# Kernel optimization log

Hardware: AMD Instinct MI355X
Metric: run time of the kernel (lower is better)

The kernel has to match this reference:

```python
import jax, jax.numpy as jnp
import numpy as np
from jax import lax

HID = 2048; NK = 16; NV = 32; DK = 128; DV = 128; KSZ = 4; CHUNK = 64; S = 2048
KEY_DIM = NK * DK; VAL_DIM = NV * DV; CONV_DIM = 2 * KEY_DIM + VAL_DIM
EPS = 1e-6


def l2norm(x, eps=1e-6):
    return x * lax.rsqrt((x * x).sum(-1, keepdims=True) + eps)


def chunk_gated_delta_rule(q, k, v, g, beta, chunk=CHUNK):
    # q,k: [B,S,Hv,DK]; v: [B,S,Hv,DV]; g,beta: [B,S,Hv]
    q = l2norm(q); k = l2norm(k)  # use_qk_l2norm_in_kernel=True
    q, k, v = (jnp.swapaxes(x, 1, 2) for x in (q, k, v))  # [B,H,S,D]
    g = jnp.swapaxes(g, 1, 2); beta = jnp.swapaxes(beta, 1, 2)  # [B,H,S]
    B, H, Ssz, Dk = k.shape; Dv = v.shape[-1]
    N = Ssz // chunk  # seq_len chosen divisible by chunk -> pad is no-op
    q = q * (Dk ** -0.5)
    vb = v * beta[..., None]
    kb = k * beta[..., None]
    rs = lambda x: x.reshape(B, H, N, chunk, x.shape[-1])
    q, k, v, kb, vb = map(rs, (q, k, v, kb, vb))
    g = jnp.cumsum(g.reshape(B, H, N, chunk), axis=-1)
    tril = jnp.tril(jnp.ones((chunk, chunk), bool))
    stril = jnp.tril(jnp.ones((chunk, chunk), bool), -1)
    diff = jnp.where(tril, g[..., :, None] - g[..., None, :], 0.0)
    decay_mask = jnp.where(tril, jnp.exp(diff), 0.0)  # [B,H,N,C,C]
    attn = jnp.where(stril, -(kb @ jnp.swapaxes(k, -1, -2)) * decay_mask, 0.0)
    # UT (WY) transform: sequential row updates, scan over in-chunk index
    def ut_body(a, i):
        row = jnp.take(a, i, axis=-2)  # [B,H,N,C]
        new = row + jnp.einsum('bhnk,bhnkj->bhnj', row, a)
        return a.at[:, :, :, i, :].set(new), None
    attn, _ = lax.scan(ut_body, attn, jnp.arange(1, chunk))
    attn = attn + jnp.eye(chunk, dtype=attn.dtype)
    u = attn @ vb                                   # [B,H,N,C,DV]
    kcd = attn @ (kb * jnp.exp(g)[..., None])       # [B,H,N,C,DK]
    init = jnp.zeros((B, H, Dk, Dv), q.dtype)
    def step(state, inp):
        q_i, k_i, u_i, kcd_i, g_i, dm_i = inp
        scores = (q_i @ jnp.swapaxes(k_i, -1, -2)) * dm_i
        v_new = u_i - kcd_i @ state
        inter = (q_i * jnp.exp(g_i)[..., None]) @ state
        o = inter + scores @ v_new
        gl = g_i[..., -1]  # [B,H]
        state = state * jnp.exp(gl)[..., None, None] + jnp.einsum(
            'bhcd,bhce->bhde', k_i * jnp.exp(gl[..., None] - g_i)[..., None], v_new)
        return state, o
    mv = lambda x: jnp.moveaxis(x, 2, 0)
    _, out = lax.scan(step, init, (mv(q), mv(k), mv(u), mv(kcd), mv(g), mv(decay_mask)))
    out = jnp.moveaxis(out, 0, 2).reshape(B, H, Ssz, Dv)
    return jnp.swapaxes(out, 1, 2)  # [B,S,H,DV]


def setup_inputs() -> dict:
    key = jax.random.key(0)
    ks = jax.random.split(key, 8)
    return {
        'hidden_states': jax.random.normal(ks[0], (S, HID), jnp.float32),
        'W_qkv': jax.random.normal(ks[1], (CONV_DIM, HID), jnp.float32) * 0.02,
        'W_z': jax.random.normal(ks[2], (VAL_DIM, HID), jnp.float32) * 0.02,
        'W_a': jax.random.normal(ks[3], (NV, HID), jnp.float32) * 0.02,
        'W_b': jax.random.normal(ks[4], (NV, HID), jnp.float32) * 0.02,
        'conv_w': jax.random.normal(ks[5], (CONV_DIM, 1, KSZ), jnp.float32) * 0.1,
        'dt_bias': jnp.ones((NV,), jnp.float32),
        'A_log': jnp.log(jax.random.uniform(ks[6], (NV,), jnp.float32, 0.1, 16.0)),
        'norm_w': jnp.ones((DV,), jnp.float32),
        'W_out': jax.random.normal(ks[7], (HID, VAL_DIM), jnp.float32) * 0.02,
    }


def reference(hidden_states, W_qkv, W_z, W_a, W_b, conv_w, dt_bias, A_log, norm_w, W_out):
    x = hidden_states  # [S, HID]
    mixed = x @ W_qkv.T  # [S, CONV_DIM]
    z = (x @ W_z.T).reshape(-1, DV)  # [S*NV, DV]
    a = x @ W_a.T  # [S, NV]
    b = x @ W_b.T
    # causal depthwise conv1d (torch pads K-1 both sides then slices [:S])
    conv = lax.conv_general_dilated(
        mixed.T[None], conv_w, (1,), [(KSZ - 1, 0)],
        dimension_numbers=('NCH', 'OIH', 'NCH'), feature_group_count=CONV_DIM)
    mixed = jax.nn.silu(conv[0].T)  # [S, CONV_DIM]
    q = mixed[:, :KEY_DIM].reshape(1, S, NK, DK)
    k = mixed[:, KEY_DIM:2 * KEY_DIM].reshape(1, S, NK, DK)
    v = mixed[:, 2 * KEY_DIM:].reshape(1, S, NV, DV)
    beta = jax.nn.sigmoid(b)[None]  # [1,S,NV]
    g = (-jnp.exp(A_log) * jax.nn.softplus(a + dt_bias))[None]  # [1,S,NV]
    ratio = NV // NK
    q = jnp.repeat(q, ratio, axis=2)
    k = jnp.repeat(k, ratio, axis=2)
    core = chunk_gated_delta_rule(q, k, v, g, beta)  # [1,S,NV,DV]
    h = core.reshape(-1, DV)  # [S*NV, DV]
    var = jnp.mean(h * h, axis=-1, keepdims=True)
    h = h * lax.rsqrt(var + EPS) * norm_w
    h = h * jax.nn.silu(z)
    out = h.reshape(S, VAL_DIM) @ W_out.T  # [S, HID]
    return out
```

## Files before the change

### kernel.cpp

```cpp
#include <hip/hip_runtime.h>
#include <hip/hip_bf16.h>
#include <math.h>

#define S_LEN   2048
#define HIDDIM  2048
#define NKH     16
#define NVH     32
#define DKD     128
#define DVD     128
#define CCH     64
#define NCHK    32
#define KEY_DIM 2048
#define VAL_DIM 4096
#define CONV_DIM 8192

#define PA_LDS_BYTES (16384 + 16384 + 32768 + 4096 + 4096 + 256 + 256 + 256)
#define PB_LDS_BYTES ((8192+8192+4096+8192+2048+1024+1024)*2 + 64*4)
#define G256_LDS_BYTES (3 * 12288 * 2)
#define G128_LDS_BYTES (3 * 8192 * 2)

typedef __bf16 bf16x8 __attribute__((ext_vector_type(8)));
typedef float f32x4 __attribute__((ext_vector_type(4)));

__device__ __forceinline__ float sigmoid_f(float x) { return 1.f / (1.f + __expf(-x)); }
__device__ __forceinline__ float silu_f(float x) { return x * sigmoid_f(x); }
__device__ __forceinline__ ushort f2bf(float f) {
    unsigned u = __float_as_uint(f);
    u += 0x7fffu + ((u >> 16) & 1u);
    return (ushort)(u >> 16);
}
__device__ __forceinline__ float bf2f(ushort u) {
    return __uint_as_float((unsigned)u << 16);
}

#define GLL(srcp, dstp) __builtin_amdgcn_global_load_lds( \
    (const __attribute__((address_space(1))) void*)(srcp), \
    (__attribute__((address_space(3))) void*)(dstp), 16, 0, 0)

__global__ __launch_bounds__(256) void cast_kernel(
    const float* __restrict__ in, ushort* __restrict__ out, int n8)
{
    int t = blockIdx.x * 256 + threadIdx.x;
    if (t >= n8) return;
    float4 v0 = *(const float4*)(in + (size_t)t * 8);
    float4 v1 = *(const float4*)(in + (size_t)t * 8 + 4);
    union { ushort u[8]; uint4 v; } r;
    r.u[0] = f2bf(v0.x); r.u[1] = f2bf(v0.y); r.u[2] = f2bf(v0.z); r.u[3] = f2bf(v0.w);
    r.u[4] = f2bf(v1.x); r.u[5] = f2bf(v1.y); r.u[6] = f2bf(v1.z); r.u[7] = f2bf(v1.w);
    *(uint4*)(out + (size_t)t * 8) = r.v;
}

__global__ __launch_bounds__(256) void cast_ab_kernel(
    const float* __restrict__ Wa, const float* __restrict__ Wb, ushort* __restrict__ out)
{
    int t = blockIdx.x * 256 + threadIdx.x;
    int row = t >> 8;
    int c8 = (t & 255) * 8;
    union { ushort u[8]; uint4 v; } r;
    if (row < 64) {
        const float* src = (row < 32) ? (Wa + (size_t)row * HIDDIM + c8)
                                      : (Wb + (size_t)(row - 32) * HIDDIM + c8);
        float4 v0 = *(const float4*)(src);
        float4 v1 = *(const float4*)(src + 4);
        r.u[0] = f2bf(v0.x); r.u[1] = f2bf(v0.y); r.u[2] = f2bf(v0.z); r.u[3] = f2bf(v0.w);
        r.u[4] = f2bf(v1.x); r.u[5] = f2bf(v1.y); r.u[6] = f2bf(v1.z); r.u[7] = f2bf(v1.w);
    } else {
        r.u[0] = r.u[1] = r.u[2] = r.u[3] = r.u[4] = r.u[5] = r.u[6] = r.u[7] = 0;
    }
    *(uint4*)(out + (size_t)t * 8) = r.v;
}

__global__ __launch_bounds__(512, 2) void gemm256_kernel(
    const ushort* __restrict__ A, const ushort* __restrict__ B,
    float* __restrict__ C0, float* __restrict__ C1,
    int K, int NSPLIT, int ldc0, int ldc1)
{
    extern __shared__ ushort g2s[];
    const int tid = threadIdx.x;
    const int wv = tid >> 6, ln = tid & 63;
    const int wm = wv >> 2, wn = wv & 3;
    const int lrow = ln & 15, lkg = ln >> 4;
    const int bm = blockIdx.y * 128, bn = blockIdx.x * 256;

    int soffA, soffB[2];
    {
        int l = tid & 63;
        soffA = (((tid >> 6) * 16) + (l & 15)) * K + (l >> 4) * 8;
#pragma unroll
        for (int j = 0; j < 2; ++j) {
            int g = tid + j * 512;
            int lg = g & 63;
            soffB[j] = (((g >> 6) * 16) + (lg & 15)) * K + (lg >> 4) * 8;
        }
    }
    const ushort* Abase = A + (size_t)bm * K;
    const ushort* Bbase = B + (size_t)bn * K;

    f32x4 acc[4][4];
#pragma unroll
    for (int m = 0; m < 4; ++m)
#pragma unroll
        for (int n = 0; n < 4; ++n) {
            f32x4 z = {0.f, 0.f, 0.f, 0.f};
            acc[m][n] = z;
        }

#define G256_STAGE(bb, k0) do {                                            \
        ushort* bufA_ = g2s + (bb) * 12288;                                \
        ushort* bufB_ = bufA_ + 4096;                                      \
        GLL(Abase + soffA + (k0), bufA_ + (wv * 64) * 8);                  \
        _Pragma("unroll")                                                  \
        for (int j_ = 0; j_ < 2; ++j_)                                     \
            GLL(Bbase + soffB[j_] + (k0), bufB_ + (j_ * 512 + wv * 64) * 8);\
    } while (0)

    const int T = K >> 5;
    G256_STAGE(0, 0);
    G256_STAGE(1, 32);
    int bb = 0;
    for (int t = 0; t < T; ++t) {
        if (t + 1 < T) {
            asm volatile("s_waitcnt vmcnt(3)" ::: "memory");
        } else {
            asm volatile("s_waitcnt vmcnt(0)" ::: "memory");
        }
        __builtin_amdgcn_s_barrier();
        if (t + 2 < T) G256_STAGE((bb >= 1) ? (bb - 1) : (bb + 2), (t + 2) * 32);
        const ushort* LA = g2s + bb * 12288;
        const ushort* LB = LA + 4096;
        __builtin_amdgcn_s_setprio(1);
        {
            bf16x8 afv[4], bfv[4];
#pragma unroll
            for (int mf = 0; mf < 4; ++mf)
                afv[mf] = *(const bf16x8*)&LA[((wm * 4 + mf) * 64 + ln) * 8];
#pragma unroll
            for (int nf = 0; nf < 4; ++nf)
                bfv[nf] = *(const bf16x8*)&LB[((wn * 4 + nf) * 64 + ln) * 8];
#pragma unroll
            for (int mf = 0; mf < 4; ++mf)
#pragma unroll
                for (int nf = 0; nf < 4; ++nf)
                    acc[mf][nf] = __builtin_amdgcn_mfma_f32_16x16x32_bf16(
                        afv[mf], bfv[nf], acc[mf][nf], 0, 0, 0);
        }
        __builtin_amdgcn_s_setprio(0);
        bb = (bb == 2) ? 0 : bb + 1;
    }
#undef G256_STAGE

    const bool inC1 = (bn >= NSPLIT);
    float* Cp = inC1 ? C1 : C0;
    const int ldc = inC1 ? ldc1 : ldc0;
    const int cb = bn + wn * 64 - (inC1 ? NSPLIT : 0);
#pragma unroll
    for (int mf = 0; mf < 4; ++mf) {
        const int row0 = bm + wm * 64 + mf * 16 + lkg * 4;
#pragma unroll
        for (int nf = 0; nf < 4; ++nf) {
            float* cp = Cp + (size_t)row0 * ldc + cb + nf * 16 + lrow;
#pragma unroll
            for (int j = 0; j < 4; ++j) cp[(size_t)j * ldc] = acc[mf][nf][j];
        }
    }
}

__global__ __launch_bounds__(256, 2) void gemm128_kernel(
    const ushort* __restrict__ A, const ushort* __restrict__ B,
    float* __restrict__ C, int N, int K)
{
    extern __shared__ ushort g1s[];
    const int tid = threadIdx.x;
    const int wv = tid >> 6, ln = tid & 63;
    const int wm = wv >> 1, wn = wv & 1;
    const int lrow = ln & 15, lkg = ln >> 4;
    const int bm = blockIdx.y * 128, bn = blockIdx.x * 128;

    int soff[2];
#pragma unroll
    for (int j = 0; j < 2; ++j) {
        int g = tid + j * 256;
        int l = g & 63;
        soff[j] = (((g >> 6) * 16) + (l & 15)) * K + (l >> 4) * 8;
    }
    const ushort* Abase = A + (size_t)bm * K;
    const ushort* Bbase = B + (size_t)bn * K;

    f32x4 acc[4][4];
#pragma unroll
    for (int m = 0; m < 4; ++m)
#pragma unroll
        for (int n = 0; n < 4; ++n) {
            f32x4 z = {0.f, 0.f, 0.f, 0.f};
            acc[m][n] = z;
        }

#define G128_STAGE(bb, k0) do {                                            \
        ushort* bufA_ = g1s + (bb) * 8192;                                 \
        ushort* bufB_ = bufA_ + 4096;                                      \
        _Pragma("unroll")                                                  \
        for (int j_ = 0; j_ < 2; ++j_) {                                   \
            GLL(Abase + soff[j_] + (k0), bufA_ + (j_ * 256 + wv * 64) * 8);\
            GLL(Bbase + soff[j_] + (k0), bufB_ + (j_ * 256 + wv * 64) * 8);\
        }                                                                  \
    } while (0)

    const int T = K >> 5;
    G128_STAGE(0, 0);
    G128_STAGE(1, 32);
    int bb = 0;
    for (int t = 0; t < T; ++t) {
        if (t + 1 < T) {
            asm volatile("s_waitcnt vmcnt(4)" ::: "memory");
        } else {
            asm volatile("s_waitcnt vmcnt(0)" ::: "memory");
        }
        __builtin_amdgcn_s_barrier();
        if (t + 2 < T) G128_STAGE((bb >= 1) ? (bb - 1) : (bb + 2), (t + 2) * 32);
        const ushort* LA = g1s + bb * 8192;
        const ushort* LB = LA + 4096;
        __builtin_amdgcn_s_setprio(1);
        {
            bf16x8 afv[4], bfv[4];
#pragma unroll
            for (int mf = 0; mf < 4; ++mf)
                afv[mf] = *(const bf16x8*)&LA[((wm * 4 + mf) * 64 + ln) * 8];
#pragma unroll
            for (int nf = 0; nf < 4; ++nf)
                bfv[nf] = *(const bf16x8*)&LB[((wn * 4 + nf) * 64 + ln) * 8];
#pragma unroll
            for (int mf = 0; mf < 4; ++mf)
#pragma unroll
                for (int nf = 0; nf < 4; ++nf)
                    acc[mf][nf] = __builtin_amdgcn_mfma_f32_16x16x32_bf16(
                        afv[mf], bfv[nf], acc[mf][nf], 0, 0, 0);
        }
        __builtin_amdgcn_s_setprio(0);
        bb = (bb == 2) ? 0 : bb + 1;
    }
#undef G128_STAGE

#pragma unroll
    for (int mf = 0; mf < 4; ++mf) {
        const int row0 = bm + wm * 64 + mf * 16 + lkg * 4;
#pragma unroll
        for (int nf = 0; nf < 4; ++nf) {
            float* cp = C + (size_t)row0 * N + bn + wn * 64 + nf * 16 + lrow;
#pragma unroll
            for (int j = 0; j < 4; ++j) cp[(size_t)j * N] = acc[mf][nf][j];
        }
    }
}

__global__ __launch_bounds__(256) void conv_silu_kernel(
    const float* __restrict__ pre, const float* __restrict__ cw, float* __restrict__ out)
{
    int idx = blockIdx.x * 256 + threadIdx.x;
    const int NC4 = CONV_DIM / 4;
    int s = idx / NC4;
    int c = (idx % NC4) * 4;
    float w[4][4];
#pragma unroll
    for (int j = 0; j < 4; ++j) {
        float4 wj = *(const float4*)(cw + (size_t)(c + j) * 4);
        w[j][0] = wj.x; w[j][1] = wj.y; w[j][2] = wj.z; w[j][3] = wj.w;
    }
    float acc[4] = {0.f, 0.f, 0.f, 0.f};
#pragma unroll
    for (int t = 0; t < 4; ++t) {
        int ss = s - 3 + t;
        if (ss >= 0) {
            float4 x = *(const float4*)(pre + (size_t)ss * CONV_DIM + c);
            acc[0] = fmaf(x.x, w[0][t], acc[0]);
            acc[1] = fmaf(x.y, w[1][t], acc[1]);
            acc[2] = fmaf(x.z, w[2][t], acc[2]);
            acc[3] = fmaf(x.w, w[3][t], acc[3]);
        }
    }
    float4 o = make_float4(silu_f(acc[0]), silu_f(acc[1]), silu_f(acc[2]), silu_f(acc[3]));
    *(float4*)(out + (size_t)s * CONV_DIM + c) = o;
}

__global__ __launch_bounds__(256) void gb_kernel(
    const float* __restrict__ ab, const float* __restrict__ dt_bias,
    const float* __restrict__ A_log, float* __restrict__ g, float* __restrict__ beta)
{
    int idx = blockIdx.x * 256 + threadIdx.x;
    int s = idx >> 5, h = idx & 31;
    float av = ab[(size_t)s * 128 + h] + dt_bias[h];
    float sp = (av > 20.f) ? av : log1pf(__expf(av));
    g[idx] = -__expf(A_log[h]) * sp;
    beta[idx] = sigmoid_f(ab[(size_t)s * 128 + 32 + h]);
}

__global__ __launch_bounds__(256) void l2norm_kernel(
    const float* __restrict__ mixed, ushort* __restrict__ qnb, float* __restrict__ kn)
{
    int gw = (blockIdx.x * 256 + threadIdx.x) >> 6;
    int lane = threadIdx.x & 63;
    int isk = gw >= S_LEN * NKH;
    int r = gw - isk * S_LEN * NKH;
    int s = r / NKH, kh = r % NKH;
    const float* src = mixed + (size_t)s * CONV_DIM + isk * KEY_DIM + kh * DKD;
    float2 x = *(const float2*)(src + lane * 2);
    float ss = x.x * x.x + x.y * x.y;
#pragma unroll
    for (int m = 1; m < 64; m <<= 1) ss += __shfl_xor(ss, m, 64);
    float scale = rsqrtf(ss + 1e-6f);
    if (!isk) {
        scale *= 0.08838834764831843f;
        union { ushort u[2]; uint v; } p;
        p.u[0] = f2bf(x.x * scale); p.u[1] = f2bf(x.y * scale);
        *(uint*)(qnb + ((size_t)(s * NKH + kh)) * DKD + lane * 2) = p.v;
    } else {
        float* dst = kn + ((size_t)(s * NKH + kh)) * DKD + lane * 2;
        *(float2*)dst = make_float2(x.x * scale, x.y * scale);
    }
}

__global__ __launch_bounds__(256) void phaseA_kernel(
    const ushort* __restrict__ qnb, const float* __restrict__ kn,
    const float* __restrict__ mixed, const float* __restrict__ gbuf,
    const float* __restrict__ betabuf,
    float* __restrict__ u, ushort* __restrict__ kcd,
    ushort* __restrict__ scores, float* __restrict__ gcs_out,
    ushort* __restrict__ knT)
{
    extern __shared__ char pasm[];
    ushort* kb    = (ushort*)(pasm);
    ushort* qb    = (ushort*)(pasm + 16384);
    ushort* Xb    = (ushort*)(pasm + 32768);
    float*  Adiag = (float*)(pasm + 65536);
    ushort* Ab    = (ushort*)(pasm + 69632);
    float*  gcs_s = (float*)(pasm + 73728);
    float*  bet_s = (float*)(pasm + 73984);
    float*  scK_s = (float*)(pasm + 74240);
    float*  Pf    = (float*)qb;

    const int n = blockIdx.x, h = blockIdx.y, kh = h >> 1;
    const int tid = threadIdx.x;
    const int s0 = n * CCH;
    const int wv = tid >> 6, ln = tid & 63;
    const int lrow = ln & 15, lkg = ln >> 4;

    float xr[64];
    if (tid < 128) {
        const float* vp = mixed + (size_t)s0 * CONV_DIM + 2 * KEY_DIM + h * DVD + tid;
#pragma unroll
        for (int i = 0; i < 64; ++i) xr[i] = vp[(size_t)i * CONV_DIM];
    } else {
        const float* kp = kn + ((size_t)s0 * NKH + kh) * DKD + (tid - 128);
#pragma unroll
        for (int i = 0; i < 64; ++i) xr[i] = kp[(size_t)i * (NKH * DKD)];
    }

    {
        uint4 z = {0, 0, 0, 0};
#pragma unroll
        for (int i = 0; i < 8; ++i)
            *(uint4*)&Xb[(i * 256 + tid) * 8] = z;
        *(uint4*)&Ab[tid * 8] = z;
    }

    if (tid < 64) {
        float gv = gbuf[(size_t)(s0 + tid) * NVH + h];
#pragma unroll
        for (int off = 1; off < 64; off <<= 1) {
            float pv = __shfl_up(gv, off, 64);
            if (tid >= off) gv += pv;
        }
        float bv = betabuf[(size_t)(s0 + tid) * NVH + h];
        gcs_s[tid] = gv;
        bet_s[tid] = bv;
        scK_s[tid] = bv * __expf(gv);
        gcs_out[(size_t)h * S_LEN + s0 + tid] = gv;
    }

    {
        const int r = tid >> 2, c0 = (tid & 3) * 32;
        const int mbase = (((r >> 4) * 4 + (tid & 3)) * 64 + (r & 15)) * 8;
        const float* ksrc = kn + ((size_t)(s0 + r) * NKH + kh) * DKD + c0;
#pragma unroll
        for (int j0 = 0; j0 < 4; ++j0) {
            float4 v0 = *(const float4*)(ksrc + j0 * 8);
            float4 v1 = *(const float4*)(ksrc + j0 * 8 + 4);
            union { ushort us[8]; uint4 v; } p;
            p.us[0] = f2bf(v0.x); p.us[1] = f2bf(v0.y); p.us[2] = f2bf(v0.z); p.us[3] = f2bf(v0.w);
            p.us[4] = f2bf(v1.x); p.us[5] = f2bf(v1.y); p.us[6] = f2bf(v1.z); p.us[7] = f2bf(v1.w);
            *(uint4*)&kb[mbase + (j0 << 7)] = p.v;
        }
        const ushort* qsrc = qnb + ((size_t)(s0 + r) * NKH + kh) * DKD + c0;
#pragma unroll
        for (int j0 = 0; j0 < 4; ++j0) {
            uint4 v = *(const uint4*)(qsrc + j0 * 8);
            *(uint4*)&qb[mbase + (j0 << 7)] = v;
        }
    }
    __syncthreads();

    f32x4 accA[4], accQ[4];
#pragma unroll
    for (int j = 0; j < 4; ++j) {
        f32x4 z = {0.f, 0.f, 0.f, 0.f};
        accA[j] = z; accQ[j] = z;
    }
#pragma unroll
    for (int ks = 0; ks < 4; ++ks) {
        bf16x8 a_k = *(const bf16x8*)&kb[((wv * 4 + ks) * 64 + ln) * 8];
        bf16x8 a_q = *(const bf16x8*)&qb[((wv * 4 + ks) * 64 + ln) * 8];
#pragma unroll
        for (int j = 0; j < 4; ++j) {
            bf16x8 b_k = *(const bf16x8*)&kb[((j * 4 + ks) * 64 + ln) * 8];
            accA[j] = __builtin_amdgcn_mfma_f32_16x16x32_bf16(a_k, b_k, accA[j], 0, 0, 0);
            accQ[j] = __builtin_amdgcn_mfma_f32_16x16x32_bf16(a_q, b_k, accQ[j], 0, 0, 0);
        }
    }
    {
        ushort* scp = scores + (size_t)(h * NCHK + n) * (CCH * CCH);
#pragma unroll
        for (int j = 0; j < 4; ++j) {
            const int c = j * 16 + lrow;
            const float gc = gcs_s[c];
#pragma unroll
            for (int jj = 0; jj < 4; ++jj) {
                const int i = wv * 16 + lkg * 4 + jj;
                const float e = __expf(gcs_s[i] - gc);
                float sv = (i >= c) ? (accQ[j][jj] * e) : 0.f;
                scp[i * CCH + c] = f2bf(sv);
                float aval = (i > c) ? (-bet_s[i] * accA[j][jj] * e) : 0.f;
                if (j == wv) {
                    Adiag[wv * 256 + (i & 15) * 16 + lrow] = aval;
                } else if (j < wv) {
                    const int f = (wv == 1) ? 0 : ((wv == 2) ? 1 : (2 + (j >> 1)));
                    const int lk = ((j & 1) << 4) | lrow;
                    const int lane2 = (i & 15) | ((lk >> 3) << 4);
                    Ab[(f * 64 + lane2) * 8 + (lk & 7)] = f2bf(aval);
                }
            }
        }
    }
    if (tid < 128) {
#pragma unroll
        for (int i4 = 0; i4 < 16; ++i4) {
            float4 b4 = *(const float4*)&bet_s[i4 * 4];
            xr[i4 * 4 + 0] *= b4.x; xr[i4 * 4 + 1] *= b4.y;
            xr[i4 * 4 + 2] *= b4.z; xr[i4 * 4 + 3] *= b4.w;
        }
    } else {
#pragma unroll
        for (int i4 = 0; i4 < 16; ++i4) {
            float4 b4 = *(const float4*)&scK_s[i4 * 4];
            xr[i4 * 4 + 0] *= b4.x; xr[i4 * 4 + 1] *= b4.y;
            xr[i4 * 4 + 2] *= b4.z; xr[i4 * 4 + 3] *= b4.w;
        }
    }
    __syncthreads();

    const int ct = tid >> 4, lct = tid & 15;
#pragma unroll
    for (int s = 0; s < 4; ++s) {
        float y[16];
        float pr[16];
        if (s > 0) {
#pragma unroll
            for (int r = 0; r < 16; ++r) pr[r] = Pf[r * 256 + tid];
        } else {
#pragma unroll
            for (int r = 0; r < 16; ++r) pr[r] = 0.f;
        }
#pragma unroll
        for (int r = 0; r < 16; ++r) {
            float acc = xr[s * 16 + r] + pr[r];
#pragma unroll
            for (int k4 = 0; k4 < 16; k4 += 4) {
                if (k4 < r) {
                    float4 a4 = *(const float4*)&Adiag[s * 256 + r * 16 + k4];
                    if (k4 + 0 < r) acc = fmaf(a4.x, y[k4 + 0], acc);
                    if (k4 + 1 < r) acc = fmaf(a4.y, y[k4 + 1], acc);
                    if (k4 + 2 < r) acc = fmaf(a4.z, y[k4 + 2], acc);
                    if (k4 + 3 < r) acc = fmaf(a4.w, y[k4 + 3], acc);
                }
            }
            y[r] = acc;
        }
        if (tid < 128) {
            float* up = u + (size_t)(h * NCHK + n) * (CCH * DVD) + (s * 16) * DVD + tid;
#pragma unroll
            for (int r = 0; r < 16; ++r) up[r * DVD] = y[r];
        } else {
            ushort* kp = kcd + (size_t)(h * NCHK + n) * (CCH * DKD) + (s * 16) * DKD + (tid - 128);
#pragma unroll
            for (int r = 0; r < 16; ++r) kp[r * DKD] = f2bf(y[r]);
        }
        if (s < 3) {
#pragma unroll
            for (int half = 0; half < 2; ++half) {
                union { ushort us[8]; uint4 v; } p;
#pragma unroll
                for (int e = 0; e < 8; ++e) p.us[e] = f2bf(y[half * 8 + e]);
                const int kg = (s & 1) * 2 + half;
                *(uint4*)&Xb[(((s >> 1) * 16 + ct) * 64 + (kg * 16 + lct)) * 8] = p.v;
            }
            __syncthreads();
            const int snx = s + 1;
            const int nT2 = (snx + 1) >> 1;
            f32x4 accP[4];
#pragma unroll
            for (int ctl = 0; ctl < 4; ++ctl) {
                f32x4 z = {0.f, 0.f, 0.f, 0.f};
                accP[ctl] = z;
            }
#pragma unroll
            for (int t2 = 0; t2 < 2; ++t2) {
                if (t2 < nT2) {
                    const int f = (snx == 1) ? 0 : ((snx == 2) ? 1 : (2 + t2));
                    bf16x8 a = *(const bf16x8*)&Ab[(f * 64 + ln) * 8];
#pragma unroll
                    for (int ctl = 0; ctl < 4; ++ctl) {
                        bf16x8 b = *(const bf16x8*)&Xb[((t2 * 16 + wv * 4 + ctl) * 64 + ln) * 8];
                        accP[ctl] = __builtin_amdgcn_mfma_f32_16x16x32_bf16(a, b, accP[ctl], 0, 0, 0);
                    }
                }
            }
#pragma unroll
            for (int ctl = 0; ctl < 4; ++ctl)
#pragma unroll
                for (int jj = 0; jj < 4; ++jj)
                    Pf[(lkg * 4 + jj) * 256 + wv * 64 + ctl * 16 + lrow] = accP[ctl][jj];
            __syncthreads();
        }
    }

    if (!(h & 1)) {
        const int dk = tid >> 1, ch = (tid & 1) * 32;
        ushort* dst = knT + ((size_t)(kh * NCHK + n) * DKD + dk) * CCH + ch;
        const int kpart = ((dk >> 5) * 64) * 8 + (((dk >> 3) & 3) << 4) * 8 + (dk & 7);
#pragma unroll
        for (int j0 = 0; j0 < 32; j0 += 8) {
            union { ushort us[8]; uint4 v; } p;
#pragma unroll
            for (int j = 0; j < 8; ++j) {
                const int row = ch + j0 + j;
                p.us[j] = kb[((row >> 4) * 4 * 64 + (row & 15)) * 8 + kpart];
            }
            *(uint4*)(dst + j0) = p.v;
        }
    }
}

__global__ __launch_bounds__(256) void phaseB_kernel(
    const ushort* __restrict__ qnb, const ushort* __restrict__ knT,
    const float* __restrict__ u, const ushort* __restrict__ kcd,
    const ushort* __restrict__ sc, const float* __restrict__ gcs,
    float* __restrict__ obuf)
{
    extern __shared__ ushort smu[];
    ushort* qorg  = smu;
    ushort* kcorg = smu + 8192;
    ushort* scorg = smu + 16384;
    ushort* kTorg = smu + 20480;
    ushort* storg = smu + 28672;
    ushort* vnorg = smu + 30720;
    ushort* vnsorg= smu + 31744;
    float* gcs_s  = (float*)(smu + 32768);

    const int h = blockIdx.x;
    const int dvb = blockIdx.y;
    const int d0 = dvb * 16;
    const int kh = h >> 1;
    const int tid = threadIdx.x;
    const int wv = tid >> 6, ln = tid & 63;
    const int lrow = ln & 15, lkg = ln >> 4;

    for (int i = tid; i < 2048 / 8; i += 256) {
        uint4 z = {0, 0, 0, 0};
        *(uint4*)&storg[i * 8] = z;
    }

    const int q_lane  = lrow * (NKH * DKD) + kh * DKD + wv * 32 + lkg * 8;
    const int kc_lane = lrow * DKD + wv * 32 + lkg * 8;
    const int st_lane = ((tid >> 7) * 16 + lrow) * 64 + ((tid >> 6) & 1) * 32 + lkg * 8;
    const int dst_e   = wv * 512;

    f32x4 accS0 = {0.f, 0.f, 0.f, 0.f}, accS1 = {0.f, 0.f, 0.f, 0.f};

    for (int n = 0; n < NCHK; ++n) {
        const int s0 = n * CCH;
        const ushort* qsrc  = qnb + (size_t)s0 * (NKH * DKD);
        const ushort* kcsrc = kcd + (size_t)(h * NCHK + n) * (CCH * DKD);
        const ushort* scsrc = sc  + (size_t)(h * NCHK + n) * (CCH * CCH);
        const ushort* kTsrc = knT + (size_t)(kh * NCHK + n) * (DKD * CCH);
#pragma unroll
        for (int r = 0; r < 4; ++r) {
            GLL(qsrc + q_lane + r * 32768, &qorg[r * 2048 + dst_e]);
            GLL(kcsrc + kc_lane + r * 2048, &kcorg[r * 2048 + dst_e]);
            GLL(kTsrc + st_lane + r * 2048, &kTorg[r * 2048 + dst_e]);
        }
#pragma unroll
        for (int r = 0; r < 2; ++r)
            GLL(scsrc + st_lane + r * 2048, &scorg[r * 2048 + dst_e]);
        if (tid < 64) gcs_s[tid] = gcs[(size_t)h * S_LEN + s0 + tid];
        __syncthreads();

        f32x4 accv = {0.f, 0.f, 0.f, 0.f};
        f32x4 acco = {0.f, 0.f, 0.f, 0.f};
#pragma unroll
        for (int ks = 0; ks < 4; ++ks) {
            bf16x8 b_st = *(const bf16x8*)&storg[(ks * 64 + ln) * 8];
            bf16x8 a_kc = *(const bf16x8*)&kcorg[((wv * 4 + ks) * 64 + ln) * 8];
            bf16x8 a_q  = *(const bf16x8*)&qorg[((wv * 4 + ks) * 64 + ln) * 8];
            accv = __builtin_amdgcn_mfma_f32_16x16x32_bf16(a_kc, b_st, accv, 0, 0, 0);
            acco = __builtin_amdgcn_mfma_f32_16x16x32_bf16(a_q, b_st, acco, 0, 0, 0);
        }
        const float* up = u + (size_t)(h * NCHK + n) * (CCH * DVD)
                            + (wv * 16 + lkg * 4) * DVD + d0 + lrow;
        float u0 = up[0], u1 = up[DVD], u2 = up[2 * DVD], u3 = up[3 * DVD];
        const float gl = gcs_s[63];
        float vn0 = u0 - accv[0], vn1 = u1 - accv[1];
        float vn2 = u2 - accv[2], vn3 = u3 - accv[3];
        {
            const int row = wv * 16 + lkg * 4;
            float g0 = gcs_s[row], g1 = gcs_s[row + 1], g2 = gcs_s[row + 2], g3 = gcs_s[row + 3];
            acco[0] *= __expf(g0); acco[1] *= __expf(g1);
            acco[2] *= __expf(g2); acco[3] *= __expf(g3);
            const int eb = ((wv >> 1) * 64 + ((wv & 1) * 2 + (lkg >> 1)) * 16 + lrow) * 8
                         + (lkg & 1) * 4;
            union { ushort u2a[4]; uint2 v; } pa, pb;
            pa.u2a[0] = f2bf(vn0); pa.u2a[1] = f2bf(vn1);
            pa.u2a[2] = f2bf(vn2); pa.u2a[3] = f2bf(vn3);
            pb.u2a[0] = f2bf(vn0 * __expf(gl - g0)); pb.u2a[1] = f2bf(vn1 * __expf(gl - g1));
            pb.u2a[2] = f2bf(vn2 * __expf(gl - g2)); pb.u2a[3] = f2bf(vn3 * __expf(gl - g3));
            *(uint2*)&vnorg[eb] = pa.v;
            *(uint2*)&vnsorg[eb] = pb.v;
        }
        __syncthreads();

#pragma unroll
        for (int ks = 0; ks < 2; ++ks) {
            bf16x8 a_sc = *(const bf16x8*)&scorg[((wv * 2 + ks) * 64 + ln) * 8];
            bf16x8 b_vn = *(const bf16x8*)&vnorg[(ks * 64 + ln) * 8];
            acco = __builtin_amdgcn_mfma_f32_16x16x32_bf16(a_sc, b_vn, acco, 0, 0, 0);
        }
        float* op = obuf + (size_t)(s0 + wv * 16 + lkg * 4) * VAL_DIM + h * DVD + d0 + lrow;
        op[0] = acco[0]; op[VAL_DIM] = acco[1];
        op[2 * VAL_DIM] = acco[2]; op[3 * VAL_DIM] = acco[3];

        const float egl = __expf(gl);
        accS0 *= egl; accS1 *= egl;
#pragma unroll
        for (int ks = 0; ks < 2; ++ks) {
            bf16x8 a_vs = *(const bf16x8*)&vnsorg[(ks * 64 + ln) * 8];
            bf16x8 b_k0 = *(const bf16x8*)&kTorg[(((wv * 2 + 0) * 2 + ks) * 64 + ln) * 8];
            bf16x8 b_k1 = *(const bf16x8*)&kTorg[(((wv * 2 + 1) * 2 + ks) * 64 + ln) * 8];
            accS0 = __builtin_amdgcn_mfma_f32_16x16x32_bf16(a_vs, b_k0, accS0, 0, 0, 0);
            accS1 = __builtin_amdgcn_mfma_f32_16x16x32_bf16(a_vs, b_k1, accS1, 0, 0, 0);
        }
#pragma unroll
        for (int j = 0; j < 4; ++j) {
            storg[(wv * 64 + ((lrow >> 3)) * 16 + lkg * 4 + j) * 8 + (lrow & 7)] = f2bf(accS0[j]);
            storg[(wv * 64 + (2 + (lrow >> 3)) * 16 + lkg * 4 + j) * 8 + (lrow & 7)] = f2bf(accS1[j]);
        }
        __syncthreads();
    }
}

__global__ __launch_bounds__(256) void norm_kernel(
    const float* __restrict__ obuf, const float* __restrict__ z,
    const float* __restrict__ nw, ushort* __restrict__ hbuf)
{
    int row = (blockIdx.x * 256 + threadIdx.x) >> 6;
    int lane = threadIdx.x & 63;
    float2 x = *(const float2*)(obuf + (size_t)row * DVD + lane * 2);
    float ss = x.x * x.x + x.y * x.y;
#pragma unroll
    for (int m = 1; m < 64; m <<= 1) ss += __shfl_xor(ss, m, 64);
    float scale = rsqrtf(ss * (1.f / DVD) + 1e-6f);
    float2 zz = *(const float2*)(z + (size_t)row * DVD + lane * 2);
    float2 w2 = *(const float2*)(nw + lane * 2);
    float h0 = x.x * scale * w2.x * silu_f(zz.x);
    float h1 = x.y * scale * w2.y * silu_f(zz.y);
    union { ushort u[2]; uint v; } r;
    r.u[0] = f2bf(h0); r.u[1] = f2bf(h1);
    *(uint*)(hbuf + (size_t)row * DVD + lane * 2) = r.v;
}

extern "C" void kernel_launch(void* const* d_in, const int* in_sizes, int n_in,
                              void* d_out, int out_size, void* d_ws, size_t ws_size,
                              hipStream_t stream)
{
    (void)in_sizes; (void)n_in; (void)out_size; (void)ws_size;
    const float* x      = (const float*)d_in[0];
    const float* W_qkv  = (const float*)d_in[1];
    const float* W_z    = (const float*)d_in[2];
    const float* W_a    = (const float*)d_in[3];
    const float* W_b    = (const float*)d_in[4];
    const float* conv_w = (const float*)d_in[5];
    const float* dt_b   = (const float*)d_in[6];
    const float* A_log  = (const float*)d_in[7];
    const float* norm_w = (const float*)d_in[8];
    const float* W_out  = (const float*)d_in[9];
    float* out = (float*)d_out;

    char* ws = (char*)d_ws;
    float*  mixed_pre = (float*)(ws);
    float*  u_buf     = (float*)(ws);
    ushort* kcd_buf   = (ushort*)(ws + 33554432);
    ushort* knT_buf   = (ushort*)(ws + 50331648);
    ushort* wqz       = (ushort*)(ws + 67108864);
    ushort* xb        = (ushort*)(ws + 117440512);
    float*  mixed     = (float*)(ws + 67108864);
    float*  obuf      = (float*)(ws + 67108864);
    ushort* hbuf      = (ushort*)(ws + 100663296);
    ushort* wob       = (ushort*)(ws + 117440512);
    float*  z_buf     = (float*)(ws + 134217728);
    ushort* sc_buf    = (ushort*)(ws + 167772160);
    ushort* wabb      = (ushort*)(ws + 167772160);
    float*  ab_buf    = (float*)(ws + 168296448);
    ushort* qnb       = (ushort*)(ws + 176160768);
    float*  kn        = (float*)(ws + 184549376);
    float*  g_buf     = (float*)(ws + 201326592);
    float*  bet_buf   = (float*)(ws + 201588736);
    float*  gcs_buf   = (float*)(ws + 201850880);

    hipFuncSetAttribute((const void*)phaseA_kernel,
                        hipFuncAttributeMaxDynamicSharedMemorySize, PA_LDS_BYTES);
    hipFuncSetAttribute((const void*)phaseB_kernel,
                        hipFuncAttributeMaxDynamicSharedMemorySize, PB_LDS_BYTES);
    hipFuncSetAttribute((const void*)gemm256_kernel,
                        hipFuncAttributeMaxDynamicSharedMemorySize, G256_LDS_BYTES);
    hipFuncSetAttribute((const void*)gemm128_kernel,
                        hipFuncAttributeMaxDynamicSharedMemorySize, G128_LDS_BYTES);

    dim3 blk(256);
    cast_kernel<<<(S_LEN * HIDDIM / 8) / 256, blk, 0, stream>>>(x, xb, S_LEN * HIDDIM / 8);
    cast_kernel<<<(CONV_DIM * HIDDIM / 8) / 256, blk, 0, stream>>>(W_qkv, wqz, CONV_DIM * HIDDIM / 8);
    cast_kernel<<<(VAL_DIM * HIDDIM / 8) / 256, blk, 0, stream>>>(W_z, wqz + (size_t)CONV_DIM * HIDDIM, VAL_DIM * HIDDIM / 8);
    cast_ab_kernel<<<(128 * HIDDIM / 8) / 256, blk, 0, stream>>>(W_a, W_b, wabb);
    gemm256_kernel<<<dim3((CONV_DIM + VAL_DIM) / 256, S_LEN / 128), dim3(512), G256_LDS_BYTES, stream>>>(
        xb, wqz, mixed_pre, z_buf, HIDDIM, CONV_DIM, CONV_DIM, VAL_DIM);
    gemm128_kernel<<<dim3(1, S_LEN / 128), blk, G128_LDS_BYTES, stream>>>(
        xb, wabb, ab_buf, 128, HIDDIM);
    conv_silu_kernel<<<(S_LEN * CONV_DIM / 4) / 256, blk, 0, stream>>>(mixed_pre, conv_w, mixed);
    gb_kernel<<<(S_LEN * NVH) / 256, blk, 0, stream>>>(ab_buf, dt_b, A_log, g_buf, bet_buf);
    l2norm_kernel<<<(2 * S_LEN * NKH * 64) / 256, blk, 0, stream>>>(mixed, qnb, kn);
    phaseA_kernel<<<dim3(NCHK, NVH), blk, PA_LDS_BYTES, stream>>>(
        qnb, kn, mixed, g_buf, bet_buf, u_buf, kcd_buf, sc_buf, gcs_buf, knT_buf);
    phaseB_kernel<<<dim3(NVH, 8), blk, PB_LDS_BYTES, stream>>>(
        qnb, knT_buf, u_buf, kcd_buf, sc_buf, gcs_buf, obuf);
    cast_kernel<<<(HIDDIM * VAL_DIM / 8) / 256, blk, 0, stream>>>(W_out, wob, HIDDIM * VAL_DIM / 8);
    norm_kernel<<<(S_LEN * NVH * 64) / 256, blk, 0, stream>>>(obuf, z_buf, norm_w, hbuf);
    gemm128_kernel<<<dim3(HIDDIM / 128, S_LEN / 128), blk, G128_LDS_BYTES, stream>>>(
        hbuf, wob, out, HIDDIM, VAL_DIM);
}
```

Measured before the change: 491.8 us.

## Fuse conv+SiLU with q/k L2 norm and store z and core output in bf16

Merges the causal depthwise conv/SiLU kernel with the q/k L2-normalisation kernel into one per-token kernel that keeps q/k in LDS, normalises them and writes v to a compact buffer. This removes one launch and a full fp32 round trip of the mixed tensor. Separately, the z projection output and the chunked-delta-rule output are now stored as bf16, halving their write and read traffic in the GEMM epilogue, phase B and the norm kernel. The cost is extra rounding of z and the attention output before the gated RMSNorm, and one block per token with limited parallelism inside each block.

```diff
diff --git a/kernel.cpp b/kernel.cpp
--- a/kernel.cpp
+++ b/kernel.cpp
@@ -72,8 +72,8 @@
 
 __global__ __launch_bounds__(512, 2) void gemm256_kernel(
     const ushort* __restrict__ A, const ushort* __restrict__ B,
-    float* __restrict__ C0, float* __restrict__ C1,
-    int K, int NSPLIT, int ldc0, int ldc1)
+    float* __restrict__ C0, void* __restrict__ C1,
+    int K, int NSPLIT, int ldc0, int ldc1, int c1bf16)
 {
     extern __shared__ ushort g2s[];
     const int tid = threadIdx.x;
@@ -150,17 +150,41 @@
 #undef G256_STAGE
 
     const bool inC1 = (bn >= NSPLIT);
-    float* Cp = inC1 ? C1 : C0;
-    const int ldc = inC1 ? ldc1 : ldc0;
-    const int cb = bn + wn * 64 - (inC1 ? NSPLIT : 0);
-#pragma unroll
-    for (int mf = 0; mf < 4; ++mf) {
-        const int row0 = bm + wm * 64 + mf * 16 + lkg * 4;
-#pragma unroll
-        for (int nf = 0; nf < 4; ++nf) {
-            float* cp = Cp + (size_t)row0 * ldc + cb + nf * 16 + lrow;
-#pragma unroll
-            for (int j = 0; j < 4; ++j) cp[(size_t)j * ldc] = acc[mf][nf][j];
+    const int cboff = bn + wn * 64 - (inC1 ? NSPLIT : 0);
+    if (!inC1) {
+#pragma unroll
+        for (int mf = 0; mf < 4; ++mf) {
+            const int row0 = bm + wm * 64 + mf * 16 + lkg * 4;
+#pragma unroll
+            for (int nf = 0; nf < 4; ++nf) {
+                float* cp = C0 + (size_t)row0 * ldc0 + cboff + nf * 16 + lrow;
+#pragma unroll
+                for (int j = 0; j < 4; ++j) cp[(size_t)j * ldc0] = acc[mf][nf][j];
+            }
+        }
+    } else if (!c1bf16) {
+        float* C1f = (float*)C1;
+#pragma unroll
+        for (int mf = 0; mf < 4; ++mf) {
+            const int row0 = bm + wm * 64 + mf * 16 + lkg * 4;
+#pragma unroll
+            for (int nf = 0; nf < 4; ++nf) {
+                float* cp = C1f + (size_t)row0 * ldc1 + cboff + nf * 16 + lrow;
+#pragma unroll
+                for (int j = 0; j < 4; ++j) cp[(size_t)j * ldc1] = acc[mf][nf][j];
+            }
+        }
+    } else {
+        ushort* C1b = (ushort*)C1;
+#pragma unroll
+        for (int mf = 0; mf < 4; ++mf) {
+            const int row0 = bm + wm * 64 + mf * 16 + lkg * 4;
+#pragma unroll
+            for (int nf = 0; nf < 4; ++nf) {
+                ushort* cp = C1b + (size_t)row0 * ldc1 + cboff + nf * 16 + lrow;
+#pragma unroll
+                for (int j = 0; j < 4; ++j) cp[(size_t)j * ldc1] = f2bf(acc[mf][nf][j]);
+            }
         }
     }
 }
@@ -252,33 +276,72 @@
     }
 }
 
-__global__ __launch_bounds__(256) void conv_silu_kernel(
-    const float* __restrict__ pre, const float* __restrict__ cw, float* __restrict__ out)
-{
-    int idx = blockIdx.x * 256 + threadIdx.x;
-    const int NC4 = CONV_DIM / 4;
-    int s = idx / NC4;
-    int c = (idx % NC4) * 4;
-    float w[4][4];
+__global__ __launch_bounds__(256) void front_kernel(
+    const float* __restrict__ pre, const float* __restrict__ cw,
+    ushort* __restrict__ qnb, float* __restrict__ kn, float* __restrict__ vbuf)
+{
+    __shared__ float stage[4096];
+    __shared__ float sums[32];
+    __shared__ float scal[32];
+    const int s = blockIdx.x;
+    const int tid = threadIdx.x;
+
+#pragma unroll
+    for (int cg = 0; cg < 8; ++cg) {
+        const int c = cg * 1024 + tid * 4;
+        float w[4][4];
+#pragma unroll
+        for (int j = 0; j < 4; ++j) {
+            float4 wj = *(const float4*)(cw + (size_t)(c + j) * 4);
+            w[j][0] = wj.x; w[j][1] = wj.y; w[j][2] = wj.z; w[j][3] = wj.w;
+        }
+        float a0 = 0.f, a1 = 0.f, a2 = 0.f, a3 = 0.f;
+#pragma unroll
+        for (int t = 0; t < 4; ++t) {
+            int ss = s - 3 + t;
+            if (ss >= 0) {
+                float4 x = *(const float4*)(pre + (size_t)ss * CONV_DIM + c);
+                a0 = fmaf(x.x, w[0][t], a0);
+                a1 = fmaf(x.y, w[1][t], a1);
+                a2 = fmaf(x.z, w[2][t], a2);
+                a3 = fmaf(x.w, w[3][t], a3);
+            }
+        }
+        a0 = silu_f(a0); a1 = silu_f(a1); a2 = silu_f(a2); a3 = silu_f(a3);
+        if (cg < 4) {
+            float4 v4 = make_float4(a0, a1, a2, a3);
+            *(float4*)&stage[c] = v4;
+            float ss2 = a0 * a0 + a1 * a1 + a2 * a2 + a3 * a3;
+#pragma unroll
+            for (int m = 1; m < 32; m <<= 1) ss2 += __shfl_xor(ss2, m, 32);
+            if ((tid & 31) == 0) sums[c >> 7] = ss2;
+        } else {
+            *(float4*)(vbuf + (size_t)s * VAL_DIM + (c - 4096)) =
+                make_float4(a0, a1, a2, a3);
+        }
+    }
+    __syncthreads();
+    if (tid < 32) {
+        float sc = rsqrtf(sums[tid] + 1e-6f);
+        if (tid < 16) sc *= 0.08838834764831843f;
+        scal[tid] = sc;
+    }
+    __syncthreads();
 #pragma unroll
     for (int j = 0; j < 4; ++j) {
-        float4 wj = *(const float4*)(cw + (size_t)(c + j) * 4);
-        w[j][0] = wj.x; w[j][1] = wj.y; w[j][2] = wj.z; w[j][3] = wj.w;
-    }
-    float acc[4] = {0.f, 0.f, 0.f, 0.f};
-#pragma unroll
-    for (int t = 0; t < 4; ++t) {
-        int ss = s - 3 + t;
-        if (ss >= 0) {
-            float4 x = *(const float4*)(pre + (size_t)ss * CONV_DIM + c);
-            acc[0] = fmaf(x.x, w[0][t], acc[0]);
-            acc[1] = fmaf(x.y, w[1][t], acc[1]);
-            acc[2] = fmaf(x.z, w[2][t], acc[2]);
-            acc[3] = fmaf(x.w, w[3][t], acc[3]);
-        }
-    }
-    float4 o = make_float4(silu_f(acc[0]), silu_f(acc[1]), silu_f(acc[2]), silu_f(acc[3]));
-    *(float4*)(out + (size_t)s * CONV_DIM + c) = o;
+        const int c = j * 1024 + tid * 4;
+        float4 v4 = *(const float4*)&stage[c];
+        const float sc = scal[c >> 7];
+        v4.x *= sc; v4.y *= sc; v4.z *= sc; v4.w *= sc;
+        if (c < 2048) {
+            union { ushort u2[4]; uint2 v; } p;
+            p.u2[0] = f2bf(v4.x); p.u2[1] = f2bf(v4.y);
+            p.u2[2] = f2bf(v4.z); p.u2[3] = f2bf(v4.w);
+            *(uint2*)(qnb + ((size_t)(s * NKH + (c >> 7))) * DKD + (c & 127)) = p.v;
+        } else {
+            *(float4*)(kn + ((size_t)(s * NKH + ((c >> 7) - 16))) * DKD + (c & 127)) = v4;
+        }
+    }
 }
 
 __global__ __launch_bounds__(256) void gb_kernel(
@@ -293,34 +356,9 @@
     beta[idx] = sigmoid_f(ab[(size_t)s * 128 + 32 + h]);
 }
 
-__global__ __launch_bounds__(256) void l2norm_kernel(
-    const float* __restrict__ mixed, ushort* __restrict__ qnb, float* __restrict__ kn)
-{
-    int gw = (blockIdx.x * 256 + threadIdx.x) >> 6;
-    int lane = threadIdx.x & 63;
-    int isk = gw >= S_LEN * NKH;
-    int r = gw - isk * S_LEN * NKH;
-    int s = r / NKH, kh = r % NKH;
-    const float* src = mixed + (size_t)s * CONV_DIM + isk * KEY_DIM + kh * DKD;
-    float2 x = *(const float2*)(src + lane * 2);
-    float ss = x.x * x.x + x.y * x.y;
-#pragma unroll
-    for (int m = 1; m < 64; m <<= 1) ss += __shfl_xor(ss, m, 64);
-    float scale = rsqrtf(ss + 1e-6f);
-    if (!isk) {
-        scale *= 0.08838834764831843f;
-        union { ushort u[2]; uint v; } p;
-        p.u[0] = f2bf(x.x * scale); p.u[1] = f2bf(x.y * scale);
-        *(uint*)(qnb + ((size_t)(s * NKH + kh)) * DKD + lane * 2) = p.v;
-    } else {
-        float* dst = kn + ((size_t)(s * NKH + kh)) * DKD + lane * 2;
-        *(float2*)dst = make_float2(x.x * scale, x.y * scale);
-    }
-}
-
 __global__ __launch_bounds__(256) void phaseA_kernel(
     const ushort* __restrict__ qnb, const float* __restrict__ kn,
-    const float* __restrict__ mixed, const float* __restrict__ gbuf,
+    const float* __restrict__ vbuf, const float* __restrict__ gbuf,
     const float* __restrict__ betabuf,
     float* __restrict__ u, ushort* __restrict__ kcd,
     ushort* __restrict__ scores, float* __restrict__ gcs_out,
@@ -345,9 +383,9 @@
 
     float xr[64];
     if (tid < 128) {
-        const float* vp = mixed + (size_t)s0 * CONV_DIM + 2 * KEY_DIM + h * DVD + tid;
-#pragma unroll
-        for (int i = 0; i < 64; ++i) xr[i] = vp[(size_t)i * CONV_DIM];
+        const float* vp = vbuf + (size_t)s0 * VAL_DIM + h * DVD + tid;
+#pragma unroll
+        for (int i = 0; i < 64; ++i) xr[i] = vp[(size_t)i * VAL_DIM];
     } else {
         const float* kp = kn + ((size_t)s0 * NKH + kh) * DKD + (tid - 128);
 #pragma unroll
@@ -552,7 +590,7 @@
     const ushort* __restrict__ qnb, const ushort* __restrict__ knT,
     const float* __restrict__ u, const ushort* __restrict__ kcd,
     const ushort* __restrict__ sc, const float* __restrict__ gcs,
-    float* __restrict__ obuf)
+    ushort* __restrict__ obuf)
 {
     extern __shared__ ushort smu[];
     ushort* qorg  = smu;
@@ -641,9 +679,9 @@
             bf16x8 b_vn = *(const bf16x8*)&vnorg[(ks * 64 + ln) * 8];
             acco = __builtin_amdgcn_mfma_f32_16x16x32_bf16(a_sc, b_vn, acco, 0, 0, 0);
         }
-        float* op = obuf + (size_t)(s0 + wv * 16 + lkg * 4) * VAL_DIM + h * DVD + d0 + lrow;
-        op[0] = acco[0]; op[VAL_DIM] = acco[1];
-        op[2 * VAL_DIM] = acco[2]; op[3 * VAL_DIM] = acco[3];
+        ushort* op = obuf + (size_t)(s0 + wv * 16 + lkg * 4) * VAL_DIM + h * DVD + d0 + lrow;
+        op[0] = f2bf(acco[0]); op[VAL_DIM] = f2bf(acco[1]);
+        op[2 * VAL_DIM] = f2bf(acco[2]); op[3 * VAL_DIM] = f2bf(acco[3]);
 
         const float egl = __expf(gl);
         accS0 *= egl; accS1 *= egl;
@@ -665,20 +703,22 @@
 }
 
 __global__ __launch_bounds__(256) void norm_kernel(
-    const float* __restrict__ obuf, const float* __restrict__ z,
+    const ushort* __restrict__ obuf, const ushort* __restrict__ z,
     const float* __restrict__ nw, ushort* __restrict__ hbuf)
 {
     int row = (blockIdx.x * 256 + threadIdx.x) >> 6;
     int lane = threadIdx.x & 63;
-    float2 x = *(const float2*)(obuf + (size_t)row * DVD + lane * 2);
-    float ss = x.x * x.x + x.y * x.y;
+    uint ov = *(const uint*)(obuf + (size_t)row * DVD + lane * 2);
+    float x0 = bf2f((ushort)ov), x1 = bf2f((ushort)(ov >> 16));
+    float ss = x0 * x0 + x1 * x1;
 #pragma unroll
     for (int m = 1; m < 64; m <<= 1) ss += __shfl_xor(ss, m, 64);
     float scale = rsqrtf(ss * (1.f / DVD) + 1e-6f);
-    float2 zz = *(const float2*)(z + (size_t)row * DVD + lane * 2);
+    uint zv = *(const uint*)(z + (size_t)row * DVD + lane * 2);
+    float z0 = bf2f((ushort)zv), z1 = bf2f((ushort)(zv >> 16));
     float2 w2 = *(const float2*)(nw + lane * 2);
-    float h0 = x.x * scale * w2.x * silu_f(zz.x);
-    float h1 = x.y * scale * w2.y * silu_f(zz.y);
+    float h0 = x0 * scale * w2.x * silu_f(z0);
+    float h1 = x1 * scale * w2.y * silu_f(z1);
     union { ushort u[2]; uint v; } r;
     r.u[0] = f2bf(h0); r.u[1] = f2bf(h1);
     *(uint*)(hbuf + (size_t)row * DVD + lane * 2) = r.v;
@@ -708,11 +748,11 @@
     ushort* knT_buf   = (ushort*)(ws + 50331648);
     ushort* wqz       = (ushort*)(ws + 67108864);
     ushort* xb        = (ushort*)(ws + 117440512);
-    float*  mixed     = (float*)(ws + 67108864);
-    float*  obuf      = (float*)(ws + 67108864);
+    float*  vbuf      = (float*)(ws + 67108864);
+    ushort* obuf      = (ushort*)(ws + 67108864);
     ushort* hbuf      = (ushort*)(ws + 100663296);
     ushort* wob       = (ushort*)(ws + 117440512);
-    float*  z_buf     = (float*)(ws + 134217728);
+    ushort* z_buf     = (ushort*)(ws + 134217728);
     ushort* sc_buf    = (ushort*)(ws + 167772160);
     ushort* wabb      = (ushort*)(ws + 167772160);
     float*  ab_buf    = (float*)(ws + 168296448);
@@ -737,14 +777,13 @@
     cast_kernel<<<(VAL_DIM * HIDDIM / 8) / 256, blk, 0, stream>>>(W_z, wqz + (size_t)CONV_DIM * HIDDIM, VAL_DIM * HIDDIM / 8);
     cast_ab_kernel<<<(128 * HIDDIM / 8) / 256, blk, 0, stream>>>(W_a, W_b, wabb);
     gemm256_kernel<<<dim3((CONV_DIM + VAL_DIM) / 256, S_LEN / 128), dim3(512), G256_LDS_BYTES, stream>>>(
-        xb, wqz, mixed_pre, z_buf, HIDDIM, CONV_DIM, CONV_DIM, VAL_DIM);
+        xb, wqz, mixed_pre, (void*)z_buf, HIDDIM, CONV_DIM, CONV_DIM, VAL_DIM, 1);
     gemm128_kernel<<<dim3(1, S_LEN / 128), blk, G128_LDS_BYTES, stream>>>(
         xb, wabb, ab_buf, 128, HIDDIM);
-    conv_silu_kernel<<<(S_LEN * CONV_DIM / 4) / 256, blk, 0, stream>>>(mixed_pre, conv_w, mixed);
+    front_kernel<<<S_LEN, blk, 0, stream>>>(mixed_pre, conv_w, qnb, kn, vbuf);
     gb_kernel<<<(S_LEN * NVH) / 256, blk, 0, stream>>>(ab_buf, dt_b, A_log, g_buf, bet_buf);
-    l2norm_kernel<<<(2 * S_LEN * NKH * 64) / 256, blk, 0, stream>>>(mixed, qnb, kn);
     phaseA_kernel<<<dim3(NCHK, NVH), blk, PA_LDS_BYTES, stream>>>(
-        qnb, kn, mixed, g_buf, bet_buf, u_buf, kcd_buf, sc_buf, gcs_buf, knT_buf);
+        qnb, kn, vbuf, g_buf, bet_buf, u_buf, kcd_buf, sc_buf, gcs_buf, knT_buf);
     phaseB_kernel<<<dim3(NVH, 8), blk, PB_LDS_BYTES, stream>>>(
         qnb, knT_buf, u_buf, kcd_buf, sc_buf, gcs_buf, obuf);
     cast_kernel<<<(HIDDIM * VAL_DIM / 8) / 256, blk, 0, stream>>>(W_out, wob, HIDDIM * VAL_DIM / 8);
```

Result: faster. 478.6 us (-2.7%).
